# Optimization experiments

Hardware: AMD Instinct MI355X
Metric: run time of the kernel (lower is better)

Reference implementation:

```python
import jax, jax.numpy as jnp
from jax import lax
import numpy as np

T, B, D = 512, 256, 32
H, OUT = 512, 32


def setup_inputs() -> dict:
    key = jax.random.key(0)
    ks = jax.random.split(key, 8)
    s_ih = 1.0 / np.sqrt(H)
    return {
        "y": jax.random.normal(ks[0], (T, B, D), dtype=jnp.float32),
        "t": jax.random.uniform(ks[1], (T, B), dtype=jnp.float32),
        # PyTorch LSTM params: gate order i, f, g, o
        "W_ih": jax.random.uniform(ks[2], (4 * H, D + 1), minval=-s_ih, maxval=s_ih, dtype=jnp.float32),
        "W_hh": jax.random.uniform(ks[3], (4 * H, H), minval=-s_ih, maxval=s_ih, dtype=jnp.float32),
        "b_ih": jax.random.uniform(ks[4], (4 * H,), minval=-s_ih, maxval=s_ih, dtype=jnp.float32),
        "b_hh": jax.random.uniform(ks[5], (4 * H,), minval=-s_ih, maxval=s_ih, dtype=jnp.float32),
        "W_lin": jax.random.uniform(ks[6], (OUT, H), minval=-s_ih, maxval=s_ih, dtype=jnp.float32),
        "b_lin": jax.random.uniform(ks[7], (OUT,), minval=-s_ih, maxval=s_ih, dtype=jnp.float32),
    }


def reference(y, t, W_ih, W_hh, b_ih, b_hh, W_lin, b_lin):
    # y: (T, B, D); t: (T, B). Concatenate time as an extra input feature.
    y_in = jnp.concatenate([y, t[..., None]], axis=-1)  # (T, B, D+1)
    # Reverse-time traversal, as in the original Python loop.
    x_rev = y_in[::-1]
    # Precompute input projection + both biases for all steps at once.
    x_proj = jnp.einsum("tbd,gd->tbg", x_rev, W_ih) + (b_ih + b_hh)  # (T, B, 4H)
    h0 = jnp.zeros((y.shape[1], W_hh.shape[1]), dtype=y.dtype)

    def step(carry, xp):
        h, c = carry
        gates = xp + h @ W_hh.T  # (B, 4H)
        i, f, g, o = jnp.split(gates, 4, axis=-1)
        c = jax.nn.sigmoid(f) * c + jax.nn.sigmoid(i) * jnp.tanh(g)
        h = jax.nn.sigmoid(o) * jnp.tanh(c)
        return (h, c), None

    (h_last, _), _ = lax.scan(step, (h0, h0), x_proj)
    # Linear applied to the final step's output (seq dim kept, len 1).
    return h_last[None] @ W_lin.T + b_lin  # (1, B, OUT)
```

## Files before the change

kernel.cpp:

```cpp
#include <hip/hip_runtime.h>


#define T_STEPS 512
#define BATCH   256
#define HID     512
#define RSTRIDE 1168
#define GSTRIDE 1024
#define HOFF    (64 * RSTRIDE)
#define LDS_BYTES (96 * RSTRIDE)
#define IMG_BYTES (BATCH * GSTRIDE)

typedef __attribute__((ext_vector_type(8))) short short8;
typedef __attribute__((ext_vector_type(4))) float f32x4;

__device__ __forceinline__ unsigned short f2bf(float f) {
  union { float f; unsigned u; } v; v.f = f;
  unsigned r = v.u + 0x7FFFu + ((v.u >> 16) & 1u);
  return (unsigned short)(r >> 16);
}
__device__ __forceinline__ float sigm(float x) { return 1.f / (1.f + __expf(-x)); }
__device__ __forceinline__ float tanh_f(float x) { return 1.f - 2.f / (__expf(2.f * x) + 1.f); }

__global__ void __launch_bounds__(256, 1)
lstm_persist(const float* __restrict__ y, const float* __restrict__ tin,
             const float* __restrict__ Wih, const float* __restrict__ Whh,
             const float* __restrict__ bih, const float* __restrict__ bhh,
             unsigned char* __restrict__ img,
             float* __restrict__ hf32,
             int* __restrict__ flags)
{
  __shared__ __align__(16) unsigned char sm[LDS_BYTES];
  const int tid  = threadIdx.x;
  const int wave = tid >> 6, lane = tid & 63;
  const int bid  = blockIdx.x;
  const int wg_m = bid & 7;
  const int m0   = wg_m << 5;
  const int u0   = (bid >> 3) << 4;

  {
    const int c = tid >> 2, part = tid & 3;
    const int rg = ((c & 3) << 9) + u0 + (c >> 2);
    const float* whrow = Whh + (size_t)rg * HID;
    const int k0 = part << 7;
    const float4* src = (const float4*)(whrow + k0);
    #pragma unroll
    for (int i = 0; i < 32; ++i) {
      float4 f = src[i];
      uint2 p2;
      p2.x = (unsigned)f2bf(f.x) | ((unsigned)f2bf(f.y) << 16);
      p2.y = (unsigned)f2bf(f.z) | ((unsigned)f2bf(f.w) << 16);
      *(uint2*)&sm[c * RSTRIDE + ((k0 + i * 4) << 1)] = p2;
    }
    if (part == 3) {
      const float* wirow = Wih + (size_t)rg * 33;
      for (int d = 0; d < 32; d += 2) {
        unsigned p = (unsigned)f2bf(wirow[d]) | ((unsigned)f2bf(wirow[d + 1]) << 16);
        *(unsigned*)&sm[c * RSTRIDE + 1024 + (d << 1)] = p;
      }
      *(unsigned short*)&sm[c * RSTRIDE + 1088] = f2bf(wirow[32]);
      *(unsigned short*)&sm[c * RSTRIDE + 1090] = 0;
      *(unsigned*)&sm[c * RSTRIDE + 1092] = 0;
      uint4 z; z.x = z.y = z.z = z.w = 0;
      *(uint4*)&sm[c * RSTRIDE + 1096] = z;
      *(uint4*)&sm[c * RSTRIDE + 1112] = z;
      *(uint4*)&sm[c * RSTRIDE + 1128] = z;
      *(uint4*)&sm[c * RSTRIDE + 1144] = z;
    }
  }
  if (tid < 128) {
    int row = tid >> 2, i = tid & 3;
    if (i < 3) {
      uint4 z; z.x = z.y = z.z = z.w = 0;
      *(uint4*)&sm[HOFF + row * RSTRIDE + 1104 + i * 16] = z;
    }
  }

  const int cl   = (wave << 4) + (lane & 15);
  const int rg_l = ((cl & 3) << 9) + u0 + (cl >> 2);
  const float bias = bih[rg_l] + bhh[rg_l];
  const int ug   = u0 + (cl >> 2);
  const int g    = lane & 3;
  const int arow = lane & 15;
  const int kbyl = (lane >> 4) << 4;
  const int rowbase = ((g >> 1) << 4) + ((lane >> 4) << 2) + ((g & 1) << 1);
  float c0 = 0.f, c1 = 0.f;
  int* const own_flag = flags + bid * 16;

  const int hrow = tid >> 3, hl8 = tid & 7;

  __syncthreads();

  for (int s = 0; s < T_STEPS; ++s) {
    {
      const int tt = (T_STEPS - 1) - s;
      if (tid < 128) {
        const int row = tid >> 2, part = tid & 3;
        const int b = m0 + row;
        const float* ysrc = y + (((size_t)tt * BATCH + b) << 5) + (part << 3);
        float4 f0 = ((const float4*)ysrc)[0];
        float4 f1 = ((const float4*)ysrc)[1];
        uint4 p;
        p.x = (unsigned)f2bf(f0.x) | ((unsigned)f2bf(f0.y) << 16);
        p.y = (unsigned)f2bf(f0.z) | ((unsigned)f2bf(f0.w) << 16);
        p.z = (unsigned)f2bf(f1.x) | ((unsigned)f2bf(f1.y) << 16);
        p.w = (unsigned)f2bf(f1.z) | ((unsigned)f2bf(f1.w) << 16);
        *(uint4*)&sm[HOFF + row * RSTRIDE + 1024 + (part << 4)] = p;
        if (part == 3) {
          float tv = tin[(size_t)tt * BATCH + b];
          uint4 tz; tz.x = (unsigned)f2bf(tv); tz.y = tz.z = tz.w = 0;
          *(uint4*)&sm[HOFF + row * RSTRIDE + 1088] = tz;
        }
      }
    }
    if (s > 0) {
      if (wave == 0) {
        int* p = flags + ((((lane & 31) << 3) | wg_m) << 4);
        while (true) {
          int v = __hip_atomic_load(p, __ATOMIC_RELAXED, __HIP_MEMORY_SCOPE_AGENT);
          if (__all(v >= s)) break;
          __builtin_amdgcn_s_sleep(1);
        }
      }
      __syncthreads();
    }
    {
      const unsigned char* gsrc = img + (size_t)(s & 1) * IMG_BYTES + (size_t)(m0 + hrow) * GSTRIDE;
      unsigned long long v[16];
      #pragma unroll
      for (int i = 0; i < 16; ++i)
        v[i] = __hip_atomic_load((const unsigned long long*)(gsrc + (hl8 << 3) + (i << 6)),
                                 __ATOMIC_RELAXED, __HIP_MEMORY_SCOPE_AGENT);
      #pragma unroll
      for (int i = 0; i < 16; ++i)
        *(unsigned long long*)&sm[HOFF + hrow * RSTRIDE + (hl8 << 3) + (i << 6)] = v[i];
    }
    __syncthreads();

    f32x4 acc0 = {0.f, 0.f, 0.f, 0.f}, acc1 = {0.f, 0.f, 0.f, 0.f};
    #pragma unroll
    for (int ks = 0; ks < 18; ++ks) {
      const int kB = (ks << 6) + kbyl;
      short8 a0 = *(const short8*)&sm[HOFF + arow * RSTRIDE + kB];
      short8 a1 = *(const short8*)&sm[HOFF + (arow + 16) * RSTRIDE + kB];
      short8 bb = *(const short8*)&sm[cl * RSTRIDE + kB];
      acc0 = __builtin_amdgcn_mfma_f32_16x16x32_bf16(a0, bb, acc0, 0, 0, 0);
      acc1 = __builtin_amdgcn_mfma_f32_16x16x32_bf16(a1, bb, acc1, 0, 0, 0);
    }

    float vals[8];
    #pragma unroll
    for (int r = 0; r < 4; ++r) { vals[r] = acc0[r] + bias; vals[4 + r] = acc1[r] + bias; }
    float sh1[8], sh2[8], sh3[8];
    #pragma unroll
    for (int j = 0; j < 8; ++j) {
      sh1[j] = __shfl_xor(vals[j], 1);
      sh2[j] = __shfl_xor(vals[j], 2);
      sh3[j] = __shfl_xor(vals[j], 3);
    }
    float iv0, fv0, gv0, ov0, iv1, fv1, gv1, ov1;
    if (g == 0)      { iv0=vals[0]; fv0=sh1[0]; gv0=sh2[0]; ov0=sh3[0];
                       iv1=vals[1]; fv1=sh1[1]; gv1=sh2[1]; ov1=sh3[1]; }
    else if (g == 1) { iv0=sh1[2];  fv0=vals[2];gv0=sh3[2]; ov0=sh2[2];
                       iv1=sh1[3];  fv1=vals[3];gv1=sh3[3]; ov1=sh2[3]; }
    else if (g == 2) { iv0=sh2[4];  fv0=sh3[4]; gv0=vals[4];ov0=sh1[4];
                       iv1=sh2[5];  fv1=sh3[5]; gv1=vals[5];ov1=sh1[5]; }
    else             { iv0=sh3[6];  fv0=sh2[6]; gv0=sh1[6]; ov0=vals[6];
                       iv1=sh3[7];  fv1=sh2[7]; gv1=sh1[7]; ov1=vals[7]; }

    c0 = sigm(fv0) * c0 + sigm(iv0) * tanh_f(gv0);
    float h0 = sigm(ov0) * tanh_f(c0);
    c1 = sigm(fv1) * c1 + sigm(iv1) * tanh_f(gv1);
    float h1 = sigm(ov1) * tanh_f(c1);

    {
      unsigned char* gnext = img + (size_t)((s + 1) & 1) * IMG_BYTES;
      const int b0 = m0 + rowbase, b1 = b0 + 1;
      __hip_atomic_store((unsigned short*)(gnext + (size_t)b0 * GSTRIDE + (ug << 1)),
                         f2bf(h0), __ATOMIC_RELAXED, __HIP_MEMORY_SCOPE_AGENT);
      __hip_atomic_store((unsigned short*)(gnext + (size_t)b1 * GSTRIDE + (ug << 1)),
                         f2bf(h1), __ATOMIC_RELAXED, __HIP_MEMORY_SCOPE_AGENT);
      if (s == T_STEPS - 1) {
        hf32[((size_t)b0 << 9) + ug] = h0;
        hf32[((size_t)b1 << 9) + ug] = h1;
      }
    }

    __syncthreads();
    if (tid == 0)
      __hip_atomic_store(own_flag, s + 1, __ATOMIC_RELAXED, __HIP_MEMORY_SCOPE_AGENT);
  }
}

__global__ void __launch_bounds__(64)
out_proj(const float* __restrict__ hf, const float* __restrict__ Wl,
         const float* __restrict__ bl, float* __restrict__ out)
{
  const int b = blockIdx.x, l = threadIdx.x;
  const int o = l & 31, half = l >> 5;
  const float4* hrow = (const float4*)(hf + ((size_t)b << 9) + (half << 8));
  const float4* wrow = (const float4*)(Wl + ((size_t)o << 9) + (half << 8));
  float acc = 0.f;
  #pragma unroll 8
  for (int j = 0; j < 64; ++j) {
    float4 hv = hrow[j], wv = wrow[j];
    acc += hv.x * wv.x + hv.y * wv.y + hv.z * wv.z + hv.w * wv.w;
  }
  acc += __shfl_xor(acc, 32);
  if (l < 32) out[(b << 5) + o] = acc + bl[o];
}

extern "C" void kernel_launch(void* const* d_in, const int* in_sizes, int n_in,
                              void* d_out, int out_size, void* d_ws, size_t ws_size,
                              hipStream_t stream) {
  const float* y    = (const float*)d_in[0];
  const float* tin  = (const float*)d_in[1];
  const float* Wih  = (const float*)d_in[2];
  const float* Whh  = (const float*)d_in[3];
  const float* bih  = (const float*)d_in[4];
  const float* bhh  = (const float*)d_in[5];
  const float* Wlin = (const float*)d_in[6];
  const float* blin = (const float*)d_in[7];
  float* out = (float*)d_out;

  unsigned char* ws = (unsigned char*)d_ws;
  unsigned char* img = ws;
  float* hf32 = (float*)(ws + 524288);
  int* flags  = (int*)(ws + 1048576);

  hipMemsetAsync(img, 0, IMG_BYTES, stream);
  hipMemsetAsync(flags, 0, 16384, stream);

  void* args[] = { (void*)&y, (void*)&tin, (void*)&Wih, (void*)&Whh,
                   (void*)&bih, (void*)&bhh, (void*)&img, (void*)&hf32, (void*)&flags };
  hipLaunchCooperativeKernel((const void*)lstm_persist, dim3(256), dim3(256),
                             args, 0, stream);
  out_proj<<<dim3(256), dim3(64), 0, stream>>>(hf32, Wlin, blin, out);
}
```

Measured before the change: 1.802 ms.

## Replace per-block flags with tag bits embedded in bf16 hidden-state words

```diff
diff --git a/kernel.cpp b/kernel.cpp
--- a/kernel.cpp
+++ b/kernel.cpp
@@ -21,13 +21,18 @@
 __device__ __forceinline__ float sigm(float x) { return 1.f / (1.f + __expf(-x)); }
 __device__ __forceinline__ float tanh_f(float x) { return 1.f - 2.f / (__expf(2.f * x) + 1.f); }
 
+__device__ __forceinline__ void barrier_nodrain() {
+  asm volatile("s_waitcnt lgkmcnt(0)" ::: "memory");
+  __builtin_amdgcn_s_barrier();
+  __builtin_amdgcn_sched_barrier(0);
+}
+
 __global__ void __launch_bounds__(256, 1)
 lstm_persist(const float* __restrict__ y, const float* __restrict__ tin,
              const float* __restrict__ Wih, const float* __restrict__ Whh,
              const float* __restrict__ bih, const float* __restrict__ bhh,
-             unsigned char* __restrict__ img,
-             float* __restrict__ hf32,
-             int* __restrict__ flags)
+             unsigned short* __restrict__ img,
+             float* __restrict__ hf32)
 {
   __shared__ __align__(16) unsigned char sm[LDS_BYTES];
   const int tid  = threadIdx.x;
@@ -84,57 +89,72 @@
   const int kbyl = (lane >> 4) << 4;
   const int rowbase = ((g >> 1) << 4) + ((lane >> 4) << 2) + ((g & 1) << 1);
   float c0 = 0.f, c1 = 0.f;
-  int* const own_flag = flags + bid * 16;
-
   const int hrow = tid >> 3, hl8 = tid & 7;
 
   __syncthreads();
 
+  short8 bfr[18];
+  #pragma unroll
+  for (int ks = 0; ks < 18; ++ks)
+    bfr[ks] = *(const short8*)&sm[cl * RSTRIDE + (ks << 6) + kbyl];
+
+  float4 xf0, xf1; float tpf = 0.f;
+  if (tid < 128) {
+    const int row = tid >> 2, part = tid & 3;
+    const float* ysrc = y + (((size_t)(T_STEPS - 1) * BATCH + m0 + row) << 5) + (part << 3);
+    xf0 = ((const float4*)ysrc)[0];
+    xf1 = ((const float4*)ysrc)[1];
+    if (part == 3) tpf = tin[(size_t)(T_STEPS - 1) * BATCH + m0 + row];
+  }
+
   for (int s = 0; s < T_STEPS; ++s) {
+    if (tid < 128) {
+      const int row = tid >> 2, part = tid & 3;
+      uint4 p;
+      p.x = (unsigned)f2bf(xf0.x) | ((unsigned)f2bf(xf0.y) << 16);
+      p.y = (unsigned)f2bf(xf0.z) | ((unsigned)f2bf(xf0.w) << 16);
+      p.z = (unsigned)f2bf(xf1.x) | ((unsigned)f2bf(xf1.y) << 16);
+      p.w = (unsigned)f2bf(xf1.z) | ((unsigned)f2bf(xf1.w) << 16);
+      *(uint4*)&sm[HOFF + row * RSTRIDE + 1024 + (part << 4)] = p;
+      if (part == 3) {
+        uint4 tz; tz.x = (unsigned)f2bf(tpf); tz.y = tz.z = tz.w = 0;
+        *(uint4*)&sm[HOFF + row * RSTRIDE + 1088] = tz;
+      }
+    }
     {
-      const int tt = (T_STEPS - 1) - s;
-      if (tid < 128) {
-        const int row = tid >> 2, part = tid & 3;
-        const int b = m0 + row;
-        const float* ysrc = y + (((size_t)tt * BATCH + b) << 5) + (part << 3);
-        float4 f0 = ((const float4*)ysrc)[0];
-        float4 f1 = ((const float4*)ysrc)[1];
-        uint4 p;
-        p.x = (unsigned)f2bf(f0.x) | ((unsigned)f2bf(f0.y) << 16);
-        p.y = (unsigned)f2bf(f0.z) | ((unsigned)f2bf(f0.w) << 16);
-        p.z = (unsigned)f2bf(f1.x) | ((unsigned)f2bf(f1.y) << 16);
-        p.w = (unsigned)f2bf(f1.z) | ((unsigned)f2bf(f1.w) << 16);
-        *(uint4*)&sm[HOFF + row * RSTRIDE + 1024 + (part << 4)] = p;
-        if (part == 3) {
-          float tv = tin[(size_t)tt * BATCH + b];
-          uint4 tz; tz.x = (unsigned)f2bf(tv); tz.y = tz.z = tz.w = 0;
-          *(uint4*)&sm[HOFF + row * RSTRIDE + 1088] = tz;
-        }
-      }
-    }
-    if (s > 0) {
-      if (wave == 0) {
-        int* p = flags + ((((lane & 31) << 3) | wg_m) << 4);
-        while (true) {
-          int v = __hip_atomic_load(p, __ATOMIC_RELAXED, __HIP_MEMORY_SCOPE_AGENT);
-          if (__all(v >= s)) break;
-          __builtin_amdgcn_s_sleep(1);
-        }
-      }
-      __syncthreads();
-    }
-    {
-      const unsigned char* gsrc = img + (size_t)(s & 1) * IMG_BYTES + (size_t)(m0 + hrow) * GSTRIDE;
-      unsigned long long v[16];
-      #pragma unroll
-      for (int i = 0; i < 16; ++i)
-        v[i] = __hip_atomic_load((const unsigned long long*)(gsrc + (hl8 << 3) + (i << 6)),
-                                 __ATOMIC_RELAXED, __HIP_MEMORY_SCOPE_AGENT);
-      #pragma unroll
-      for (int i = 0; i < 16; ++i)
-        *(unsigned long long*)&sm[HOFF + hrow * RSTRIDE + (hl8 << 3) + (i << 6)] = v[i];
-    }
-    __syncthreads();
+      const unsigned char* gsrc = (const unsigned char*)img + (size_t)(s & 1) * IMG_BYTES
+                                + (size_t)(m0 + hrow) * GSTRIDE + (hl8 << 3);
+      unsigned char* const ldst = &sm[HOFF + hrow * RSTRIDE + (hl8 << 3)];
+      const unsigned long long wantm = ((s >> 1) & 1) ? 0x0001000100010001ULL : 0ULL;
+      unsigned miss = 0xFFFFu;
+      while (true) {
+        unsigned long long v[16];
+        #pragma unroll
+        for (int i = 0; i < 16; ++i)
+          if (miss & (1u << i))
+            v[i] = __hip_atomic_load((const unsigned long long*)(gsrc + (i << 6)),
+                                     __ATOMIC_RELAXED, __HIP_MEMORY_SCOPE_AGENT);
+        #pragma unroll
+        for (int i = 0; i < 16; ++i)
+          if ((miss & (1u << i)) &&
+              (v[i] & 0x0001000100010001ULL) == wantm) {
+            *(unsigned long long*)(ldst + (i << 6)) = v[i];
+            miss &= ~(1u << i);
+          }
+        if (miss == 0) break;
+        __builtin_amdgcn_s_sleep(1);
+      }
+    }
+    barrier_nodrain();
+
+    if (tid < 128 && s + 1 < T_STEPS) {
+      const int row = tid >> 2, part = tid & 3;
+      const int tt = (T_STEPS - 2) - s;
+      const float* ysrc = y + (((size_t)tt * BATCH + m0 + row) << 5) + (part << 3);
+      xf0 = ((const float4*)ysrc)[0];
+      xf1 = ((const float4*)ysrc)[1];
+      if (part == 3) tpf = tin[(size_t)tt * BATCH + m0 + row];
+    }
 
     f32x4 acc0 = {0.f, 0.f, 0.f, 0.f}, acc1 = {0.f, 0.f, 0.f, 0.f};
     #pragma unroll
@@ -142,9 +162,8 @@
       const int kB = (ks << 6) + kbyl;
       short8 a0 = *(const short8*)&sm[HOFF + arow * RSTRIDE + kB];
       short8 a1 = *(const short8*)&sm[HOFF + (arow + 16) * RSTRIDE + kB];
-      short8 bb = *(const short8*)&sm[cl * RSTRIDE + kB];
-      acc0 = __builtin_amdgcn_mfma_f32_16x16x32_bf16(a0, bb, acc0, 0, 0, 0);
-      acc1 = __builtin_amdgcn_mfma_f32_16x16x32_bf16(a1, bb, acc1, 0, 0, 0);
+      acc0 = __builtin_amdgcn_mfma_f32_16x16x32_bf16(a0, bfr[ks], acc0, 0, 0, 0);
+      acc1 = __builtin_amdgcn_mfma_f32_16x16x32_bf16(a1, bfr[ks], acc1, 0, 0, 0);
     }
 
     float vals[8];
@@ -173,21 +192,22 @@
     float h1 = sigm(ov1) * tanh_f(c1);
 
     {
-      unsigned char* gnext = img + (size_t)((s + 1) & 1) * IMG_BYTES;
+      const unsigned tagbit = ((unsigned)(s + 1) >> 1) & 1u;
+      unsigned short* gnext = img + (size_t)((s + 1) & 1) * (IMG_BYTES / 2);
       const int b0 = m0 + rowbase, b1 = b0 + 1;
-      __hip_atomic_store((unsigned short*)(gnext + (size_t)b0 * GSTRIDE + (ug << 1)),
-                         f2bf(h0), __ATOMIC_RELAXED, __HIP_MEMORY_SCOPE_AGENT);
-      __hip_atomic_store((unsigned short*)(gnext + (size_t)b1 * GSTRIDE + (ug << 1)),
-                         f2bf(h1), __ATOMIC_RELAXED, __HIP_MEMORY_SCOPE_AGENT);
+      unsigned short w0 = (unsigned short)((f2bf(h0) & 0xFFFEu) | tagbit);
+      unsigned short w1 = (unsigned short)((f2bf(h1) & 0xFFFEu) | tagbit);
+      __hip_atomic_store(gnext + ((size_t)b0 << 9) + ug, w0,
+                         __ATOMIC_RELAXED, __HIP_MEMORY_SCOPE_AGENT);
+      __hip_atomic_store(gnext + ((size_t)b1 << 9) + ug, w1,
+                         __ATOMIC_RELAXED, __HIP_MEMORY_SCOPE_AGENT);
       if (s == T_STEPS - 1) {
         hf32[((size_t)b0 << 9) + ug] = h0;
         hf32[((size_t)b1 << 9) + ug] = h1;
       }
     }
 
-    __syncthreads();
-    if (tid == 0)
-      __hip_atomic_store(own_flag, s + 1, __ATOMIC_RELAXED, __HIP_MEMORY_SCOPE_AGENT);
+    barrier_nodrain();
   }
 }
 
@@ -223,15 +243,14 @@
   float* out = (float*)d_out;
 
   unsigned char* ws = (unsigned char*)d_ws;
-  unsigned char* img = ws;
+  unsigned short* img = (unsigned short*)ws;
   float* hf32 = (float*)(ws + 524288);
-  int* flags  = (int*)(ws + 1048576);
-
-  hipMemsetAsync(img, 0, IMG_BYTES, stream);
-  hipMemsetAsync(flags, 0, 16384, stream);
+
+  hipMemsetAsync(ws, 0x00, IMG_BYTES, stream);
+  hipMemsetAsync(ws + IMG_BYTES, 0x01, IMG_BYTES, stream);
 
   void* args[] = { (void*)&y, (void*)&tin, (void*)&Wih, (void*)&Whh,
-                   (void*)&bih, (void*)&bhh, (void*)&img, (void*)&hf32, (void*)&flags };
+                   (void*)&bih, (void*)&bhh, (void*)&img, (void*)&hf32 };
   hipLaunchCooperativeKernel((const void*)lstm_persist, dim3(256), dim3(256),
                              args, 0, stream);
   out_proj<<<dim3(256), dim3(64), 0, stream>>>(hf32, Wlin, blin, out);
```

After: 3.964 ms. +120.0%, slower.
